# Performance work log

Hardware: AMD Instinct MI355X
Metric: run time of the kernel (lower is better)

The kernel has to match this reference:

```python
import jax, jax.numpy as jnp
import numpy as np

B, N, C, H = 2, 2048, 768, 12
HD = C // H
SCALE = HD ** -0.5


def setup_inputs() -> dict:
    key = jax.random.key(0)
    k1, k2, k3, k4 = jax.random.split(key, 4)
    return {
        "x": jax.random.normal(k1, (B, N, C), dtype=jnp.float32),
        "qkv_w": jax.random.normal(k2, (3 * C, C), dtype=jnp.float32) * (C ** -0.5),
        "proj_w": jax.random.normal(k3, (C, C), dtype=jnp.float32) * (C ** -0.5),
        "proj_b": jax.random.normal(k4, (C,), dtype=jnp.float32) * 0.01,
    }


def reference(x, qkv_w, proj_w, proj_b):
    b, n, c = x.shape
    # qkv: Linear(dim, 3*dim, bias=False) -> (B,N,3,H,HD) -> per-tensor (B,H,N,HD)
    qkv = (x @ qkv_w.T).reshape(b, n, 3, H, HD)
    q, k, v = jnp.moveaxis(qkv, 2, 0)          # each (B,N,H,HD)
    q = q.transpose(0, 2, 1, 3)                # (B,H,N,HD)
    k = k.transpose(0, 2, 1, 3)
    v = v.transpose(0, 2, 1, 3)
    attn_logits = jnp.einsum("bhqd,bhkd->bhqk", q, k) * SCALE  # (B,H,N,N)
    attn = jax.nn.softmax(attn_logits, axis=-1)
    score = jnp.mean(attn, axis=1)             # (B,N,N) mean over heads
    # dropout p=0.0 -> identity
    out = jnp.einsum("bhqk,bhkd->bhqd", attn, v)  # (B,H,N,HD)
    out = out.transpose(0, 2, 1, 3).reshape(b, n, c)
    out = out @ proj_w.T + proj_b
    return out, score
```

## Files before the change

kernel.cpp:

```cpp
#include <hip/hip_runtime.h>
#include <cstddef>

typedef __attribute__((ext_vector_type(8))) short bf16x8;
typedef __attribute__((ext_vector_type(4))) float f32x4;

constexpr int Bb = 2, Nn = 2048, Cc = 768, Hh = 12, HDd = 64;
constexpr float QSCALE = 0.125f * 1.44269504088896340736f;

#define VMCNT(n) asm volatile("s_waitcnt vmcnt(" #n ")" ::: "memory")
#define SBAR() __builtin_amdgcn_s_barrier()

__device__ inline short f2bf(float f) {
  unsigned u = __builtin_bit_cast(unsigned, f);
  u += 0x7fff + ((u >> 16) & 1);
  return (short)(u >> 16);
}
__device__ inline unsigned cvtpk(float a, float b) {
  unsigned r;
  asm("v_cvt_pk_bf16_f32 %0, %1, %2" : "=v"(r) : "v"(a), "v"(b));
  return r;
}
__device__ inline void gl_lds16(const void* g, void* l) {
  __builtin_amdgcn_global_load_lds(
      (const __attribute__((address_space(1))) unsigned*)g,
      (__attribute__((address_space(3))) unsigned*)l, 16, 0, 0);
}
__device__ inline bf16x8 lds8(const short* p) { return *(const bf16x8*)p; }
__device__ inline bf16x8 ld_frag(const short* base, int row, int ch) {
  return *(const bf16x8*)&base[row * 64 + (((ch ^ (row & 7)) << 3))];
}

__global__ __launch_bounds__(256) void cvt3_kernel(
    const float* __restrict__ s0, const float* __restrict__ s1,
    const float* __restrict__ s2, short* __restrict__ d, int n0, int n01) {
  const int i = (blockIdx.x * 256 + threadIdx.x) * 4;
  const float* src;
  int off;
  if (i < n0) {
    src = s0; off = i;
  } else if (i < n01) {
    src = s1; off = i - n0;
  } else {
    src = s2; off = i - n01;
  }
  const float4 v = *(const float4*)&src[off];
  short4 o;
  o.x = f2bf(v.x); o.y = f2bf(v.y); o.z = f2bf(v.z); o.w = f2bf(v.w);
  *(short4*)&d[i] = o;
}

__global__ __launch_bounds__(256) void qkv_mfma(
    const short* __restrict__ A, const short* __restrict__ W,
    short* __restrict__ Qg, short* __restrict__ Kg, short* __restrict__ Vtg) {
  __shared__ short As[2 * 8192];
  __shared__ short Bs[2 * 6144];
  const int t = threadIdx.x, l = t & 63, w = t >> 6;
  const int lr = l & 15, lh = l >> 4;
  const int m0 = blockIdx.x * 128, r0 = blockIdx.y * 96;
  const int wr = w >> 1, wc = w & 1;
  f32x4 acc[4][3];
#pragma unroll
  for (int i = 0; i < 4; ++i)
#pragma unroll
    for (int j = 0; j < 3; ++j) acc[i][j] = (f32x4){0.f, 0.f, 0.f, 0.f};

  auto stage = [&](const int buf, const int kt) {
#pragma unroll
    for (int u = 0; u < 4; ++u) {
      const int cu = u * 4 + w;
      const int du = cu * 64 + l;
      const int row = du >> 3, ch = du & 7, sch = ch ^ (row & 7);
      gl_lds16(A + (size_t)(m0 + row) * Cc + kt * 64 + sch * 8,
               &As[buf * 8192 + cu * 512]);
    }
#pragma unroll
    for (int u = 0; u < 3; ++u) {
      const int cu = u * 4 + w;
      const int du = cu * 64 + l;
      const int row = du >> 3, ch = du & 7, sch = ch ^ (row & 7);
      gl_lds16(W + (size_t)(r0 + row) * Cc + kt * 64 + sch * 8,
               &Bs[buf * 6144 + cu * 512]);
    }
  };
  auto compute = [&](const int buf) {
    const short* Ab = As + buf * 8192;
    const short* Bbp = Bs + buf * 6144;
#pragma unroll
    for (int kp = 0; kp < 2; ++kp) {
      bf16x8 af[4], bfv[3];
#pragma unroll
      for (int i = 0; i < 4; ++i)
        af[i] = ld_frag(Ab, wr * 64 + i * 16 + lr, kp * 4 + lh);
#pragma unroll
      for (int j = 0; j < 3; ++j)
        bfv[j] = ld_frag(Bbp, wc * 48 + j * 16 + lr, kp * 4 + lh);
      __builtin_amdgcn_s_setprio(1);
#pragma unroll
      for (int i = 0; i < 4; ++i)
#pragma unroll
        for (int j = 0; j < 3; ++j)
          acc[i][j] = __builtin_amdgcn_mfma_f32_16x16x32_bf16(
              af[i], bfv[j], acc[i][j], 0, 0, 0);
      __builtin_amdgcn_s_setprio(0);
    }
  };

  stage(0, 0);
#pragma unroll 1
  for (int kk = 0; kk < 10; kk += 2) {
    stage(1, kk + 1);
    VMCNT(7); SBAR();
    compute(0);
    SBAR();
    stage(0, kk + 2);
    VMCNT(7); SBAR();
    compute(1);
    SBAR();
  }
  stage(1, 11);
  VMCNT(7); SBAR();
  compute(0);
  SBAR();
  VMCNT(0); SBAR();
  compute(1);

  const int which = r0 / Cc;
  const int rbase = r0 % Cc;
  const int bq = m0 >> 11;
  const int nb = (m0 & 2047) + wr * 64;
  if (which == 2) {
#pragma unroll
    for (int j = 0; j < 3; ++j) {
      const int rr = rbase + wc * 48 + j * 16 + lr;
      const int head = rr >> 6, dd = rr & 63;
      short* vp = &Vtg[(((size_t)bq * Hh + head) * HDd + dd) * Nn];
#pragma unroll
      for (int i = 0; i < 4; ++i) {
        short4 o;
        o.x = f2bf(acc[i][j][0]); o.y = f2bf(acc[i][j][1]);
        o.z = f2bf(acc[i][j][2]); o.w = f2bf(acc[i][j][3]);
        *(short4*)&vp[nb + i * 16 + lh * 4] = o;
      }
    }
  } else {
    const float scl = (which == 0) ? QSCALE : 1.0f;
    short* __restrict__ dst = (which == 0) ? Qg : Kg;
#pragma unroll
    for (int j = 0; j < 3; ++j) {
      const int rr = rbase + wc * 48 + j * 16 + lr;
      const int head = rr >> 6, dd = rr & 63;
      short* dp = &dst[((size_t)bq * Hh + head) * Nn * HDd + dd];
#pragma unroll
      for (int i = 0; i < 4; ++i)
#pragma unroll
        for (int r = 0; r < 4; ++r)
          dp[(size_t)(nb + i * 16 + lh * 4 + r) * HDd] =
              f2bf(acc[i][j][r] * scl);
    }
  }
}

__global__ __launch_bounds__(256, 3) void attn_pass1(
    const short* __restrict__ Qg, const short* __restrict__ Kg,
    const short* __restrict__ Vtg, float* __restrict__ Linv,
    short* __restrict__ OHb) {
  __shared__ short SM[4 * 4096 + 4 * 1024];
  const int t = threadIdx.x, l = t & 63, w = t >> 6;
  const int lr = l & 15, lh = l >> 4;
  const int raw = blockIdx.x;
  const int bid = (raw & 7) * 96 + (raw >> 3);
  const int q0 = (bid & 31) * 64;
  const int head = (bid >> 5) % Hh;
  const int b = bid / (32 * Hh);
  const size_t base = (size_t)b * Hh + head;
  const short* Qh = Qg + base * Nn * HDd;
  const short* Kh = Kg + base * Nn * HDd;
  const short* Vh = Vtg + base * HDd * Nn;
  const int qw = q0 + w * 16;
  const int PB = 16384 + w * 1024;

  const bf16x8 onesf = {0x3F80, 0x3F80, 0x3F80, 0x3F80,
                        0x3F80, 0x3F80, 0x3F80, 0x3F80};

  int fof[2][4], wofi[4], pof[2];
#pragma unroll
  for (int kp = 0; kp < 2; ++kp) {
#pragma unroll
    for (int i = 0; i < 4; ++i)
      fof[kp][i] = (i * 16 + lr) * 64 + (((kp * 4 + lh) ^ (lr & 7)) << 3);
    pof[kp] = lr * 64 + (((kp * 4 + lh) ^ (lr & 7)) << 3);
  }
#pragma unroll
  for (int i = 0; i < 4; ++i) {
    const int ch = 2 * i + (lh >> 1);
    wofi[i] = lr * 64 + ((ch ^ (lr & 7)) << 3) + (lh & 1) * 4;
  }

  bf16x8 qf[2];
#pragma unroll
  for (int kp = 0; kp < 2; ++kp)
    qf[kp] = *(const bf16x8*)&Qh[(size_t)(qw + lr) * HDd + kp * 32 + lh * 8];

  f32x4 accO[4], accL;
  accL = (f32x4){0.f, 0.f, 0.f, 0.f};
#pragma unroll
  for (int j = 0; j < 4; ++j) accO[j] = (f32x4){0.f, 0.f, 0.f, 0.f};

  auto stage = [&](const int buf, const int tile) {
    const short* Kt = Kh + (size_t)tile * (64 * HDd);
    const short* Vt = Vh + tile * 64;
#pragma unroll
    for (int u = 0; u < 2; ++u) {
      const int cu = u * 4 + w;
      const int du = cu * 64 + l;
      const int row = du >> 3, ch = du & 7, sch = ch ^ (row & 7);
      gl_lds16(Kt + row * 64 + sch * 8, &SM[buf * 4096 + cu * 512]);
      gl_lds16(Vt + (size_t)row * Nn + sch * 8,
               &SM[8192 + buf * 4096 + cu * 512]);
    }
  };

  auto compute = [&](const int kb) {
    const int vb = 8192 + kb;
    f32x4 sacc[4];
#pragma unroll
    for (int i = 0; i < 4; ++i) sacc[i] = (f32x4){0.f, 0.f, 0.f, 0.f};
    __builtin_amdgcn_s_setprio(1);
#pragma unroll
    for (int kp = 0; kp < 2; ++kp)
#pragma unroll
      for (int i = 0; i < 4; ++i)
        sacc[i] = __builtin_amdgcn_mfma_f32_16x16x32_bf16(
            lds8(&SM[kb + fof[kp][i]]), qf[kp], sacc[i], 0, 0, 0);
    __builtin_amdgcn_s_setprio(0);
#pragma unroll
    for (int i = 0; i < 4; ++i) {
      const float p0 = exp2f(sacc[i][0]), p1 = exp2f(sacc[i][1]);
      const float p2 = exp2f(sacc[i][2]), p3 = exp2f(sacc[i][3]);
      uint2 pk;
      pk.x = cvtpk(p0, p1);
      pk.y = cvtpk(p2, p3);
      *(uint2*)&SM[PB + wofi[i]] = pk;
    }
    __builtin_amdgcn_s_setprio(1);
#pragma unroll
    for (int kp = 0; kp < 2; ++kp) {
      const bf16x8 pa = lds8(&SM[PB + pof[kp]]);
      accL = __builtin_amdgcn_mfma_f32_16x16x32_bf16(pa, onesf, accL, 0, 0, 0);
#pragma unroll
      for (int j = 0; j < 4; ++j)
        accO[j] = __builtin_amdgcn_mfma_f32_16x16x32_bf16(
            pa, lds8(&SM[vb + fof[kp][j]]), accO[j], 0, 0, 0);
    }
    __builtin_amdgcn_s_setprio(0);
  };

  stage(0, 0);
#pragma unroll 1
  for (int it = 0; it < 30; it += 2) {
    stage(1, it + 1);
    VMCNT(4); SBAR();
    compute(0);
    SBAR();
    stage(0, it + 2);
    VMCNT(4); SBAR();
    compute(4096);
    SBAR();
  }
  stage(1, 31);
  VMCNT(4); SBAR();
  compute(0);
  SBAR();
  VMCNT(0); SBAR();
  compute(4096);

  f32x4 linvq;
#pragma unroll
  for (int r = 0; r < 4; ++r) linvq[r] = 1.0f / accL[r];
  if (lr == 0) *(f32x4*)&Linv[base * Nn + qw + 4 * lh] = linvq;
#pragma unroll
  for (int j = 0; j < 4; ++j)
#pragma unroll
    for (int r = 0; r < 4; ++r)
      OHb[((size_t)b * Nn + qw + 4 * lh + r) * Cc + head * HDd + j * 16 + lr] =
          f2bf(accO[j][r] * linvq[r]);
}

__global__ __launch_bounds__(256, 4) void score_mfma(
    const short* __restrict__ Qg, const short* __restrict__ Kg,
    const float* __restrict__ Linv, float* __restrict__ score) {
  __shared__ __align__(16) char SMraw[64 * 68 * 4];
  short* SK = (short*)SMraw;
  float* SMf = (float*)SMraw;
  const int t = threadIdx.x, l = t & 63, w = t >> 6;
  const int lr = l & 15, lh = l >> 4;
  const int raw = blockIdx.x;
  const int xcd = raw & 7, idx = raw >> 3;
  const int b = xcd >> 2;
  const int q0 = ((xcd & 3) * 8 + (idx >> 5)) * 64;
  const int kv0 = (idx & 31) * 64;
  const int qw = q0 + w * 16;

  int fof[2][4];
#pragma unroll
  for (int kp = 0; kp < 2; ++kp)
#pragma unroll
    for (int i = 0; i < 4; ++i)
      fof[kp][i] = (i * 16 + lr) * 64 + (((kp * 4 + lh) ^ (lr & 7)) << 3);

  f32x4 sc[4];
#pragma unroll
  for (int i = 0; i < 4; ++i) sc[i] = (f32x4){0.f, 0.f, 0.f, 0.f};

  auto stage = [&](const int kb, const int h) {
    const short* Kt = Kg + (((size_t)b * Hh + h) * Nn + kv0) * HDd;
#pragma unroll
    for (int u = 0; u < 2; ++u) {
      const int cu = u * 4 + w;
      const int du = cu * 64 + l;
      const int row = du >> 3, ch = du & 7, sch = ch ^ (row & 7);
      gl_lds16(Kt + row * 64 + sch * 8, &SK[kb + cu * 512]);
    }
  };
  auto ldqQ = [&](const int h, bf16x8& a0, bf16x8& a1) {
    const size_t hb = (size_t)b * Hh + h;
    a0 = *(const bf16x8*)&Qg[(hb * Nn + qw + lr) * HDd + lh * 8];
    a1 = *(const bf16x8*)&Qg[(hb * Nn + qw + lr) * HDd + 32 + lh * 8];
  };
  auto qk = [&](const int kb, const bf16x8 a0, const bf16x8 a1,
                f32x4 (&sacc)[4]) {
#pragma unroll
    for (int i = 0; i < 4; ++i) sacc[i] = (f32x4){0.f, 0.f, 0.f, 0.f};
#pragma unroll
    for (int i = 0; i < 4; ++i)
      sacc[i] = __builtin_amdgcn_mfma_f32_16x16x32_bf16(
          lds8(&SK[kb + fof[0][i]]), a0, sacc[i], 0, 0, 0);
#pragma unroll
    for (int i = 0; i < 4; ++i)
      sacc[i] = __builtin_amdgcn_mfma_f32_16x16x32_bf16(
          lds8(&SK[kb + fof[1][i]]), a1, sacc[i], 0, 0, 0);
  };
  auto expacc = [&](const f32x4 (&sacc)[4], const float lv) {
#pragma unroll
    for (int i = 0; i < 4; ++i)
#pragma unroll
      for (int r = 0; r < 4; ++r) sc[i][r] += exp2f(sacc[i][r]) * lv;
  };

  bf16x8 qA0, qA1, qB0, qB1;
  float lvA, lvB;
  f32x4 sA[4], sB[4];
  stage(0, 0);
  ldqQ(0, qA0, qA1);
  __syncthreads();
  stage(4096, 1);
  ldqQ(1, qB0, qB1);
  lvA = Linv[((size_t)b * Hh + 0) * Nn + qw + lr];
  qk(0, qA0, qA1, sA);
  __syncthreads();
#pragma unroll 1
  for (int h = 1; h < 11; h += 2) {
    stage(0, h + 1);
    ldqQ(h + 1, qA0, qA1);
    lvB = Linv[((size_t)b * Hh + h) * Nn + qw + lr];
    qk(4096, qB0, qB1, sB);
    expacc(sA, lvA);
    __syncthreads();
    stage(4096, h + 2);
    ldqQ(h + 2, qB0, qB1);
    lvA = Linv[((size_t)b * Hh + h + 1) * Nn + qw + lr];
    qk(0, qA0, qA1, sA);
    expacc(sB, lvB);
    __syncthreads();
  }
  lvB = Linv[((size_t)b * Hh + 11) * Nn + qw + lr];
  qk(4096, qB0, qB1, sB);
  expacc(sA, lvA);
  expacc(sB, lvB);
  __syncthreads();

  constexpr float invH = 1.0f / 12.0f;
#pragma unroll
  for (int i = 0; i < 4; ++i) {
    f32x4 o;
#pragma unroll
    for (int r = 0; r < 4; ++r) o[r] = sc[i][r] * invH;
    *(f32x4*)&SMf[(w * 16 + lr) * 68 + i * 16 + 4 * lh] = o;
  }
  __syncthreads();
#pragma unroll
  for (int s = 0; s < 4; ++s) {
    const int lin = t + s * 256;
    const int row = lin >> 4, ch = lin & 15;
    const f32x4 v = *(const f32x4*)&SMf[row * 68 + ch * 4];
    *(f32x4*)&score[((size_t)b * Nn + q0 + row) * Nn + kv0 + ch * 4] = v;
  }
}

__global__ __launch_bounds__(256) void proj_mfma(
    const short* __restrict__ A, const short* __restrict__ W,
    const float* __restrict__ bias, float* __restrict__ out) {
  __shared__ short As[2 * 4096];
  __shared__ short Bs[2 * 4096];
  const int t = threadIdx.x, l = t & 63, w = t >> 6;
  const int lr = l & 15, lh = l >> 4;
  const int m0 = blockIdx.x * 64, c0 = blockIdx.y * 64;
  const int wr = w >> 1, wc = w & 1;
  f32x4 acc[2][2];
#pragma unroll
  for (int i = 0; i < 2; ++i)
#pragma unroll
    for (int j = 0; j < 2; ++j) acc[i][j] = (f32x4){0.f, 0.f, 0.f, 0.f};

  auto stage = [&](const int buf, const int kt) {
#pragma unroll
    for (int u = 0; u < 2; ++u) {
      const int cu = u * 4 + w;
      const int du = cu * 64 + l;
      const int row = du >> 3, ch = du & 7, sch = ch ^ (row & 7);
      gl_lds16(A + (size_t)(m0 + row) * Cc + kt * 64 + sch * 8,
               &As[buf * 4096 + cu * 512]);
      gl_lds16(W + (size_t)(c0 + row) * Cc + kt * 64 + sch * 8,
               &Bs[buf * 4096 + cu * 512]);
    }
  };
  auto compute = [&](const int buf) {
    const short* Ab = As + buf * 4096;
    const short* Bbp = Bs + buf * 4096;
#pragma unroll
    for (int kp = 0; kp < 2; ++kp) {
      bf16x8 af[2], bfv[2];
#pragma unroll
      for (int i = 0; i < 2; ++i)
        af[i] = ld_frag(Ab, wr * 32 + i * 16 + lr, kp * 4 + lh);
#pragma unroll
      for (int j = 0; j < 2; ++j)
        bfv[j] = ld_frag(Bbp, wc * 32 + j * 16 + lr, kp * 4 + lh);
      __builtin_amdgcn_s_setprio(1);
#pragma unroll
      for (int i = 0; i < 2; ++i)
#pragma unroll
        for (int j = 0; j < 2; ++j)
          acc[i][j] = __builtin_amdgcn_mfma_f32_16x16x32_bf16(
              af[i], bfv[j], acc[i][j], 0, 0, 0);
      __builtin_amdgcn_s_setprio(0);
    }
  };

  stage(0, 0);
#pragma unroll 1
  for (int kk = 0; kk < 10; kk += 2) {
    stage(1, kk + 1);
    VMCNT(4); SBAR();
    compute(0);
    SBAR();
    stage(0, kk + 2);
    VMCNT(4); SBAR();
    compute(1);
    SBAR();
  }
  stage(1, 11);
  VMCNT(4); SBAR();
  compute(0);
  SBAR();
  VMCNT(0); SBAR();
  compute(1);

#pragma unroll
  for (int j = 0; j < 2; ++j) {
    const int c = c0 + wc * 32 + j * 16 + lr;
    const float bi = bias[c];
#pragma unroll
    for (int i = 0; i < 2; ++i)
#pragma unroll
      for (int r = 0; r < 4; ++r) {
        const int m = m0 + wr * 32 + i * 16 + lh * 4 + r;
        out[(size_t)m * Cc + c] = acc[i][j][r] + bi;
      }
  }
}

extern "C" void kernel_launch(void* const* d_in, const int* in_sizes, int n_in,
                              void* d_out, int out_size, void* d_ws,
                              size_t ws_size, hipStream_t stream) {
  const float* x = (const float*)d_in[0];
  const float* qkv_w = (const float*)d_in[1];
  const float* proj_w = (const float*)d_in[2];
  const float* proj_b = (const float*)d_in[3];

  float* out = (float*)d_out;
  float* score = out + (size_t)Bb * Nn * Cc;

  const size_t nx = (size_t)Bb * Nn * Cc;
  const size_t nwq = (size_t)3 * Cc * Cc;
  const size_t npw = (size_t)Cc * Cc;
  short* xb = (short*)d_ws;
  short* wqb = xb + nx;
  short* pwb = wqb + nwq;
  short* Qb = pwb + npw;
  short* Kb = Qb + nx;
  short* Vtb = Kb + nx;
  short* OHb = Vtb + nx;
  float* Linv = (float*)(OHb + nx);

  const int ncvt = (int)((nx + nwq + npw) / 1024);
  cvt3_kernel<<<dim3(ncvt), 256, 0, stream>>>(x, qkv_w, proj_w, xb, (int)nx,
                                              (int)(nx + nwq));
  qkv_mfma<<<dim3(32, 24), 256, 0, stream>>>(xb, wqb, Qb, Kb, Vtb);
  attn_pass1<<<dim3(768), 256, 0, stream>>>(Qb, Kb, Vtb, Linv, OHb);
  score_mfma<<<dim3(2048), 256, 0, stream>>>(Qb, Kb, Linv, score);
  proj_mfma<<<dim3(64, 12), 256, 0, stream>>>(OHb, pwb, proj_b, out);
}
```

Baseline: 125.8 us.

## Use 32x32 MFMA and 128-row query tiles in score kernel

```diff
diff --git a/kernel.cpp b/kernel.cpp
--- a/kernel.cpp
+++ b/kernel.cpp
@@ -3,6 +3,7 @@
 
 typedef __attribute__((ext_vector_type(8))) short bf16x8;
 typedef __attribute__((ext_vector_type(4))) float f32x4;
+typedef __attribute__((ext_vector_type(16))) float f32x16;
 
 constexpr int Bb = 2, Nn = 2048, Cc = 768, Hh = 12, HDd = 64;
 constexpr float QSCALE = 0.125f * 1.44269504088896340736f;
@@ -26,6 +27,12 @@
       (__attribute__((address_space(3))) unsigned*)l, 16, 0, 0);
 }
 __device__ inline bf16x8 lds8(const short* p) { return *(const bf16x8*)p; }
+__device__ inline f32x16 zero16() {
+  f32x16 z;
+#pragma unroll
+  for (int r = 0; r < 16; ++r) z[r] = 0.f;
+  return z;
+}
 __device__ inline bf16x8 ld_frag(const short* base, int row, int ch) {
   return *(const bf16x8*)&base[row * 64 + (((ch ^ (row & 7)) << 3))];
 }
@@ -289,28 +296,26 @@
 __global__ __launch_bounds__(256, 4) void score_mfma(
     const short* __restrict__ Qg, const short* __restrict__ Kg,
     const float* __restrict__ Linv, float* __restrict__ score) {
-  __shared__ __align__(16) char SMraw[64 * 68 * 4];
+  __shared__ __align__(16) char SMraw[128 * 66 * 4];
   short* SK = (short*)SMraw;
-  float* SMf = (float*)SMraw;
+  float* SOUT = (float*)SMraw;
   const int t = threadIdx.x, l = t & 63, w = t >> 6;
-  const int lr = l & 15, lh = l >> 4;
+  const int lo5 = l & 31, hi5 = l >> 5;
   const int raw = blockIdx.x;
   const int xcd = raw & 7, idx = raw >> 3;
   const int b = xcd >> 2;
-  const int q0 = ((xcd & 3) * 8 + (idx >> 5)) * 64;
+  const int q0 = ((xcd & 3) * 4 + (idx >> 5)) * 128;
   const int kv0 = (idx & 31) * 64;
-  const int qw = q0 + w * 16;
-
-  int fof[2][4];
-#pragma unroll
-  for (int kp = 0; kp < 2; ++kp)
-#pragma unroll
-    for (int i = 0; i < 4; ++i)
-      fof[kp][i] = (i * 16 + lr) * 64 + (((kp * 4 + lh) ^ (lr & 7)) << 3);
-
-  f32x4 sc[4];
-#pragma unroll
-  for (int i = 0; i < 4; ++i) sc[i] = (f32x4){0.f, 0.f, 0.f, 0.f};
+  const int qw = q0 + w * 32;
+
+  int of2[2][4];
+#pragma unroll
+  for (int i = 0; i < 2; ++i)
+#pragma unroll
+    for (int s = 0; s < 4; ++s)
+      of2[i][s] = (i * 32 + lo5) * 64 + ((((2 * s + hi5) ^ (l & 7))) << 3);
+
+  f32x16 sc0 = zero16(), sc1 = zero16();
 
   auto stage = [&](const int kb, const int h) {
     const short* Kt = Kg + (((size_t)b * Hh + h) * Nn + kv0) * HDd;
@@ -322,78 +327,66 @@
       gl_lds16(Kt + row * 64 + sch * 8, &SK[kb + cu * 512]);
     }
   };
-  auto ldqQ = [&](const int h, bf16x8& a0, bf16x8& a1) {
-    const size_t hb = (size_t)b * Hh + h;
-    a0 = *(const bf16x8*)&Qg[(hb * Nn + qw + lr) * HDd + lh * 8];
-    a1 = *(const bf16x8*)&Qg[(hb * Nn + qw + lr) * HDd + 32 + lh * 8];
-  };
-  auto qk = [&](const int kb, const bf16x8 a0, const bf16x8 a1,
-                f32x4 (&sacc)[4]) {
-#pragma unroll
-    for (int i = 0; i < 4; ++i) sacc[i] = (f32x4){0.f, 0.f, 0.f, 0.f};
-#pragma unroll
-    for (int i = 0; i < 4; ++i)
-      sacc[i] = __builtin_amdgcn_mfma_f32_16x16x32_bf16(
-          lds8(&SK[kb + fof[0][i]]), a0, sacc[i], 0, 0, 0);
-#pragma unroll
-    for (int i = 0; i < 4; ++i)
-      sacc[i] = __builtin_amdgcn_mfma_f32_16x16x32_bf16(
-          lds8(&SK[kb + fof[1][i]]), a1, sacc[i], 0, 0, 0);
-  };
-  auto expacc = [&](const f32x4 (&sacc)[4], const float lv) {
-#pragma unroll
-    for (int i = 0; i < 4; ++i)
-#pragma unroll
-      for (int r = 0; r < 4; ++r) sc[i][r] += exp2f(sacc[i][r]) * lv;
-  };
-
-  bf16x8 qA0, qA1, qB0, qB1;
-  float lvA, lvB;
-  f32x4 sA[4], sB[4];
+
   stage(0, 0);
-  ldqQ(0, qA0, qA1);
-  __syncthreads();
-  stage(4096, 1);
-  ldqQ(1, qB0, qB1);
-  lvA = Linv[((size_t)b * Hh + 0) * Nn + qw + lr];
-  qk(0, qA0, qA1, sA);
   __syncthreads();
 #pragma unroll 1
-  for (int h = 1; h < 11; h += 2) {
-    stage(0, h + 1);
-    ldqQ(h + 1, qA0, qA1);
-    lvB = Linv[((size_t)b * Hh + h) * Nn + qw + lr];
-    qk(4096, qB0, qB1, sB);
-    expacc(sA, lvA);
+  for (int h = 0; h < Hh; ++h) {
+    if (h + 1 < Hh) stage(((h + 1) & 1) * 4096, h + 1);
+    const size_t hb = (size_t)b * Hh + h;
+    bf16x8 qf0 = *(const bf16x8*)&Qg[(hb * Nn + qw + lo5) * HDd + 0 + hi5 * 8];
+    bf16x8 qf1 = *(const bf16x8*)&Qg[(hb * Nn + qw + lo5) * HDd + 16 + hi5 * 8];
+    bf16x8 qf2 = *(const bf16x8*)&Qg[(hb * Nn + qw + lo5) * HDd + 32 + hi5 * 8];
+    bf16x8 qf3 = *(const bf16x8*)&Qg[(hb * Nn + qw + lo5) * HDd + 48 + hi5 * 8];
+    const float lv = Linv[hb * Nn + qw + lo5];
+    const int kb = (h & 1) * 4096;
+    f32x16 s0 = zero16(), s1 = zero16();
+    __builtin_amdgcn_s_setprio(1);
+    s0 = __builtin_amdgcn_mfma_f32_32x32x16_bf16(lds8(&SK[kb + of2[0][0]]),
+                                                 qf0, s0, 0, 0, 0);
+    s1 = __builtin_amdgcn_mfma_f32_32x32x16_bf16(lds8(&SK[kb + of2[1][0]]),
+                                                 qf0, s1, 0, 0, 0);
+    s0 = __builtin_amdgcn_mfma_f32_32x32x16_bf16(lds8(&SK[kb + of2[0][1]]),
+                                                 qf1, s0, 0, 0, 0);
+    s1 = __builtin_amdgcn_mfma_f32_32x32x16_bf16(lds8(&SK[kb + of2[1][1]]),
+                                                 qf1, s1, 0, 0, 0);
+    s0 = __builtin_amdgcn_mfma_f32_32x32x16_bf16(lds8(&SK[kb + of2[0][2]]),
+                                                 qf2, s0, 0, 0, 0);
+    s1 = __builtin_amdgcn_mfma_f32_32x32x16_bf16(lds8(&SK[kb + of2[1][2]]),
+                                                 qf2, s1, 0, 0, 0);
+    s0 = __builtin_amdgcn_mfma_f32_32x32x16_bf16(lds8(&SK[kb + of2[0][3]]),
+                                                 qf3, s0, 0, 0, 0);
+    s1 = __builtin_amdgcn_mfma_f32_32x32x16_bf16(lds8(&SK[kb + of2[1][3]]),
+                                                 qf3, s1, 0, 0, 0);
+    __builtin_amdgcn_s_setprio(0);
+#pragma unroll
+    for (int r = 0; r < 16; ++r) {
+      sc0[r] += exp2f(s0[r]) * lv;
+      sc1[r] += exp2f(s1[r]) * lv;
+    }
     __syncthreads();
-    stage(4096, h + 2);
-    ldqQ(h + 2, qB0, qB1);
-    lvA = Linv[((size_t)b * Hh + h + 1) * Nn + qw + lr];
-    qk(0, qA0, qA1, sA);
-    expacc(sB, lvB);
-    __syncthreads();
-  }
-  lvB = Linv[((size_t)b * Hh + 11) * Nn + qw + lr];
-  qk(4096, qB0, qB1, sB);
-  expacc(sA, lvA);
-  expacc(sB, lvB);
+  }
+
+  constexpr float invH = 1.0f / 12.0f;
+  const int qrow = (w * 32 + lo5) * 66;
+#pragma unroll
+  for (int g = 0; g < 4; ++g) {
+    f32x4 o0, o1;
+#pragma unroll
+    for (int e = 0; e < 4; ++e) {
+      o0[e] = sc0[4 * g + e] * invH;
+      o1[e] = sc1[4 * g + e] * invH;
+    }
+    *(f32x4*)&SOUT[qrow + 8 * g + 4 * hi5] = o0;
+    *(f32x4*)&SOUT[qrow + 32 + 8 * g + 4 * hi5] = o1;
+  }
   __syncthreads();
-
-  constexpr float invH = 1.0f / 12.0f;
-#pragma unroll
-  for (int i = 0; i < 4; ++i) {
-    f32x4 o;
-#pragma unroll
-    for (int r = 0; r < 4; ++r) o[r] = sc[i][r] * invH;
-    *(f32x4*)&SMf[(w * 16 + lr) * 68 + i * 16 + 4 * lh] = o;
-  }
-  __syncthreads();
-#pragma unroll
-  for (int s = 0; s < 4; ++s) {
-    const int lin = t + s * 256;
-    const int row = lin >> 4, ch = lin & 15;
-    const f32x4 v = *(const f32x4*)&SMf[row * 68 + ch * 4];
-    *(f32x4*)&score[((size_t)b * Nn + q0 + row) * Nn + kv0 + ch * 4] = v;
+#pragma unroll
+  for (int s = 0; s < 8; ++s) {
+    const int unit = s * 256 + t;
+    const int row = unit >> 4, c = unit & 15;
+    const f32x4 v = *(const f32x4*)&SOUT[row * 66 + c * 4];
+    *(f32x4*)&score[((size_t)b * Nn + q0 + row) * Nn + kv0 + c * 4] = v;
   }
 }
 
@@ -508,6 +501,6 @@
                                               (int)(nx + nwq));
   qkv_mfma<<<dim3(32, 24), 256, 0, stream>>>(xb, wqb, Qb, Kb, Vtb);
   attn_pass1<<<dim3(768), 256, 0, stream>>>(Qb, Kb, Vtb, Linv, OHb);
-  score_mfma<<<dim3(2048), 256, 0, stream>>>(Qb, Kb, Linv, score);
+  score_mfma<<<dim3(1024), 256, 0, stream>>>(Qb, Kb, Linv, score);
   proj_mfma<<<dim3(64, 12), 256, 0, stream>>>(OHb, pwb, proj_b, out);
 }
```

After: 129.2 us. 1.03x slower.

## Swap score kernel wave tiling so each wave owns a kv slice

Applied to the files above, without the earlier changes.

```diff
diff --git a/kernel.cpp b/kernel.cpp
--- a/kernel.cpp
+++ b/kernel.cpp
@@ -299,18 +299,15 @@
   const int b = xcd >> 2;
   const int q0 = ((xcd & 3) * 8 + (idx >> 5)) * 64;
   const int kv0 = (idx & 31) * 64;
-  const int qw = q0 + w * 16;
-
-  int fof[2][4];
+
+  int afo[2];
 #pragma unroll
   for (int kp = 0; kp < 2; ++kp)
-#pragma unroll
-    for (int i = 0; i < 4; ++i)
-      fof[kp][i] = (i * 16 + lr) * 64 + (((kp * 4 + lh) ^ (lr & 7)) << 3);
+    afo[kp] = (w * 16 + lr) * 64 + (((kp * 4 + lh) ^ (lr & 7)) << 3);
 
   f32x4 sc[4];
 #pragma unroll
-  for (int i = 0; i < 4; ++i) sc[i] = (f32x4){0.f, 0.f, 0.f, 0.f};
+  for (int j = 0; j < 4; ++j) sc[j] = (f32x4){0.f, 0.f, 0.f, 0.f};
 
   auto stage = [&](const int kb, const int h) {
     const short* Kt = Kg + (((size_t)b * Hh + h) * Nn + kv0) * HDd;
@@ -322,70 +319,72 @@
       gl_lds16(Kt + row * 64 + sch * 8, &SK[kb + cu * 512]);
     }
   };
-  auto ldqQ = [&](const int h, bf16x8& a0, bf16x8& a1) {
+  auto ldq = [&](const int h, bf16x8 (&qf)[4][2], float (&lv)[4]) {
     const size_t hb = (size_t)b * Hh + h;
-    a0 = *(const bf16x8*)&Qg[(hb * Nn + qw + lr) * HDd + lh * 8];
-    a1 = *(const bf16x8*)&Qg[(hb * Nn + qw + lr) * HDd + 32 + lh * 8];
-  };
-  auto qk = [&](const int kb, const bf16x8 a0, const bf16x8 a1,
-                f32x4 (&sacc)[4]) {
-#pragma unroll
-    for (int i = 0; i < 4; ++i) sacc[i] = (f32x4){0.f, 0.f, 0.f, 0.f};
-#pragma unroll
-    for (int i = 0; i < 4; ++i)
-      sacc[i] = __builtin_amdgcn_mfma_f32_16x16x32_bf16(
-          lds8(&SK[kb + fof[0][i]]), a0, sacc[i], 0, 0, 0);
-#pragma unroll
-    for (int i = 0; i < 4; ++i)
-      sacc[i] = __builtin_amdgcn_mfma_f32_16x16x32_bf16(
-          lds8(&SK[kb + fof[1][i]]), a1, sacc[i], 0, 0, 0);
-  };
-  auto expacc = [&](const f32x4 (&sacc)[4], const float lv) {
-#pragma unroll
-    for (int i = 0; i < 4; ++i)
-#pragma unroll
-      for (int r = 0; r < 4; ++r) sc[i][r] += exp2f(sacc[i][r]) * lv;
-  };
-
-  bf16x8 qA0, qA1, qB0, qB1;
-  float lvA, lvB;
+#pragma unroll
+    for (int j = 0; j < 4; ++j) {
+      qf[j][0] =
+          *(const bf16x8*)&Qg[(hb * Nn + q0 + j * 16 + lr) * HDd + lh * 8];
+      qf[j][1] = *(const bf16x8*)&Qg[(hb * Nn + q0 + j * 16 + lr) * HDd + 32 +
+                                     lh * 8];
+      lv[j] = Linv[hb * Nn + q0 + j * 16 + lr];
+    }
+  };
+  auto qk = [&](const int kb, const bf16x8 (&qf)[4][2], f32x4 (&sacc)[4]) {
+    const bf16x8 af0 = lds8(&SK[kb + afo[0]]);
+    const bf16x8 af1 = lds8(&SK[kb + afo[1]]);
+    __builtin_amdgcn_s_setprio(1);
+#pragma unroll
+    for (int j = 0; j < 4; ++j) {
+      f32x4 s = (f32x4){0.f, 0.f, 0.f, 0.f};
+      s = __builtin_amdgcn_mfma_f32_16x16x32_bf16(af0, qf[j][0], s, 0, 0, 0);
+      s = __builtin_amdgcn_mfma_f32_16x16x32_bf16(af1, qf[j][1], s, 0, 0, 0);
+      sacc[j] = s;
+    }
+    __builtin_amdgcn_s_setprio(0);
+  };
+  auto expacc = [&](const f32x4 (&sacc)[4], const float (&lv)[4]) {
+#pragma unroll
+    for (int j = 0; j < 4; ++j)
+#pragma unroll
+      for (int r = 0; r < 4; ++r) sc[j][r] += exp2f(sacc[j][r]) * lv[j];
+  };
+
+  bf16x8 qA[4][2], qB[4][2];
+  float lvA[4], lvB[4];
   f32x4 sA[4], sB[4];
   stage(0, 0);
-  ldqQ(0, qA0, qA1);
+  ldq(0, qA, lvA);
   __syncthreads();
   stage(4096, 1);
-  ldqQ(1, qB0, qB1);
-  lvA = Linv[((size_t)b * Hh + 0) * Nn + qw + lr];
-  qk(0, qA0, qA1, sA);
+  qk(0, qA, sA);
   __syncthreads();
 #pragma unroll 1
   for (int h = 1; h < 11; h += 2) {
     stage(0, h + 1);
-    ldqQ(h + 1, qA0, qA1);
-    lvB = Linv[((size_t)b * Hh + h) * Nn + qw + lr];
-    qk(4096, qB0, qB1, sB);
+    ldq(h, qB, lvB);
     expacc(sA, lvA);
+    qk(4096, qB, sB);
     __syncthreads();
     stage(4096, h + 2);
-    ldqQ(h + 2, qB0, qB1);
-    lvA = Linv[((size_t)b * Hh + h + 1) * Nn + qw + lr];
-    qk(0, qA0, qA1, sA);
+    ldq(h + 1, qA, lvA);
     expacc(sB, lvB);
+    qk(0, qA, sA);
     __syncthreads();
   }
-  lvB = Linv[((size_t)b * Hh + 11) * Nn + qw + lr];
-  qk(4096, qB0, qB1, sB);
+  ldq(11, qB, lvB);
   expacc(sA, lvA);
+  qk(4096, qB, sB);
   expacc(sB, lvB);
   __syncthreads();
 
   constexpr float invH = 1.0f / 12.0f;
 #pragma unroll
-  for (int i = 0; i < 4; ++i) {
+  for (int j = 0; j < 4; ++j) {
     f32x4 o;
 #pragma unroll
-    for (int r = 0; r < 4; ++r) o[r] = sc[i][r] * invH;
-    *(f32x4*)&SMf[(w * 16 + lr) * 68 + i * 16 + 4 * lh] = o;
+    for (int r = 0; r < 4; ++r) o[r] = sc[j][r] * invH;
+    *(f32x4*)&SMf[(j * 16 + lr) * 68 + w * 16 + 4 * lh] = o;
   }
   __syncthreads();
 #pragma unroll
```

Measured after the change: 186.8 us. 1.48x slower.
